# Performance work log

Hardware: AMD Instinct MI355X
Metric: run time of the kernel (lower is better)

## Reference

```python
import jax, jax.numpy as jnp
import numpy as np

B, S, D, H = 2, 2048, 1024, 16
DK = D // H

def setup_inputs() -> dict:
    key = jax.random.key(0)
    ks = jax.random.split(key, 8)
    def lin(k):
        kw, kb = jax.random.split(k)
        w = jax.random.normal(kw, (D, D), dtype=jnp.float32) / np.sqrt(D)
        b = jax.random.normal(kb, (D,), dtype=jnp.float32) * 0.01
        return w, b
    wq, bq = lin(ks[0]); wk, bk = lin(ks[1]); wv, bv = lin(ks[2]); wo, bo = lin(ks[3])
    return {
        'q': jax.random.normal(ks[4], (B, S, D), dtype=jnp.float32),
        'k': jax.random.normal(ks[5], (B, S, D), dtype=jnp.float32),
        'v': jax.random.normal(ks[6], (B, S, D), dtype=jnp.float32),
        'mask': jnp.ones((1, 1, S, S), dtype=jnp.int32),
        'wq': wq, 'bq': bq, 'wk': wk, 'bk': bk,
        'wv': wv, 'bv': bv, 'wo': wo, 'bo': bo,
    }

def reference(q, k, v, mask, wq, bq, wk, bk, wv, bv, wo, bo):
    b, s, _ = q.shape
    # QKV projections (nn.Linear: x @ W^T + b)
    Q = (q @ wq.T + bq).reshape(b, s, H, DK).transpose(0, 2, 1, 3)  # [B,H,S,DK]
    K = (k @ wk.T + bk).reshape(b, -1, H, DK).transpose(0, 2, 1, 3)
    V = (v @ wv.T + bv).reshape(b, -1, H, DK).transpose(0, 2, 1, 3)
    scores = jnp.einsum('bhqd,bhkd->bhqk', Q, K) / np.sqrt(DK)
    # faithful to source: masked positions set to -1e-09 (tiny, as written)
    scores = jnp.where(mask == 0, jnp.float32(-1e-09), scores)
    att = jax.nn.softmax(scores, axis=-1)
    x = jnp.einsum('bhqk,bhkd->bhqd', att, V)
    x = x.transpose(0, 2, 1, 3).reshape(b, s, H * DK)
    return x @ wo.T + bo
```

## Files before the change

kernel.cpp:

```cpp
#include <hip/hip_runtime.h>
#include <stdint.h>

typedef unsigned short u16;
typedef unsigned int u32;
typedef __bf16 bf16x8 __attribute__((ext_vector_type(8)));
typedef __bf16 bf16x2 __attribute__((ext_vector_type(2)));
typedef float f32x4 __attribute__((ext_vector_type(4)));
typedef float f32x16 __attribute__((ext_vector_type(16)));
typedef unsigned short u16x4 __attribute__((ext_vector_type(4)));
typedef unsigned short u16x8 __attribute__((ext_vector_type(8)));
typedef u32 u32x4 __attribute__((ext_vector_type(4)));

#define B_ 2
#define S_ 2048
#define D_ 1024
#define H_ 16

__device__ __forceinline__ u16 f2bf(float f) {
  uint32_t u = __builtin_bit_cast(uint32_t, f);
  u += 0x7FFF + ((u >> 16) & 1);
  return (u16)(u >> 16);
}

__device__ __forceinline__ u32 pkbf(float x, float y) {
  bf16x2 t;
  t.x = (__bf16)x;
  t.y = (__bf16)y;
  return __builtin_bit_cast(u32, t);
}

__device__ __forceinline__ void pl32swap(u32& a, u32& b) {
  asm("v_permlane32_swap_b32 %0, %1" : "+v"(a), "+v"(b));
}

__device__ __forceinline__ float max3f(float a, float b, float c) {
  return fmaxf(fmaxf(a, b), c);
}

__device__ __forceinline__ void gld_lds16(const void* g, void* l) {
  __builtin_amdgcn_global_load_lds((const __attribute__((address_space(1))) void*)g,
                                   (__attribute__((address_space(3))) void*)l, 16, 0, 0);
}

__global__ void cvt_w(const float* __restrict__ wq, const float* __restrict__ wk,
                      const float* __restrict__ wv, const float* __restrict__ wo,
                      u16* __restrict__ wqb, u16* __restrict__ wkb,
                      u16* __restrict__ wvb, u16* __restrict__ wob) {
  int bid = blockIdx.x;
  const float* s;
  u16* d;
  int base;
  if (bid < 1024)       { s = wq; d = wqb; base = bid; }
  else if (bid < 2048)  { s = wk; d = wkb; base = bid - 1024; }
  else if (bid < 3072)  { s = wv; d = wvb; base = bid - 2048; }
  else                  { s = wo; d = wob; base = bid - 3072; }
  int i = (base * 256 + threadIdx.x) * 4;
  float4 f = *(const float4*)(s + i);
  u16x4 o;
  o.x = f2bf(f.x); o.y = f2bf(f.y); o.z = f2bf(f.z); o.w = f2bf(f.w);
  *(u16x4*)(d + i) = o;
}

template <int EPI, bool A_FP32, int BN>
__device__ __forceinline__ void gemm_body(const void* __restrict__ Ap, const u16* __restrict__ W,
                                          const float* __restrict__ bias, void* __restrict__ Cp,
                                          float scale, int m0, int n0) {
  constexpr int K = 1024;
  constexpr int N = 1024;
  constexpr int NFR = BN / 32;
  __shared__ __align__(16) u16 As[128 * 64];
  __shared__ __align__(16) u16 Ws[BN * 64];
  const int tid = threadIdx.x;
  const int lane = tid & 63, wid = tid >> 6;
  const int wm = wid >> 1, wn = wid & 1;
  const int l15 = lane & 15, l4 = lane >> 4;

  f32x4 acc[4][NFR] = {};

  float4 areg[8];
  auto loadA = [&](int kt) {
    if (A_FP32) {
      const float* Af = (const float*)Ap;
#pragma unroll
      for (int i = 0; i < 4; ++i) {
        int c = i * 256 + tid;
        int row = c >> 3, col8 = c & 7;
        const float* src = Af + (size_t)(m0 + row) * K + kt * 64 + col8 * 8;
        areg[2 * i]     = *(const float4*)(src);
        areg[2 * i + 1] = *(const float4*)(src + 4);
      }
    }
  };
  auto writeA = [&]() {
#pragma unroll
    for (int i = 0; i < 4; ++i) {
      int c = i * 256 + tid;
      int row = c >> 3, col8 = c & 7;
      u16x8 o;
      o[0] = f2bf(areg[2 * i].x);     o[1] = f2bf(areg[2 * i].y);
      o[2] = f2bf(areg[2 * i].z);     o[3] = f2bf(areg[2 * i].w);
      o[4] = f2bf(areg[2 * i + 1].x); o[5] = f2bf(areg[2 * i + 1].y);
      o[6] = f2bf(areg[2 * i + 1].z); o[7] = f2bf(areg[2 * i + 1].w);
      *(u16x8*)((char*)As + row * 128 + ((col8 << 4) ^ ((row & 7) << 4))) = o;
    }
  };

  loadA(0);
  for (int kt = 0; kt < K / 64; ++kt) {
    __syncthreads();
    if (A_FP32) {
      writeA();
    } else {
      const u16* Ab = (const u16*)Ap;
#pragma unroll
      for (int i = 0; i < 4; ++i) {
        int c = i * 256 + tid;
        int row = c >> 3;
        int scb = ((c & 7) << 4) ^ ((row & 7) << 4);
        gld_lds16(Ab + (size_t)(m0 + row) * K + (size_t)kt * 64 + (scb >> 1),
                  (char*)As + (size_t)c * 16);
      }
    }
#pragma unroll
    for (int i = 0; i < BN / 32; ++i) {
      int c = i * 256 + tid;
      int row = c >> 3;
      int scb = ((c & 7) << 4) ^ ((row & 7) << 4);
      gld_lds16(W + (size_t)(n0 + row) * K + (size_t)kt * 64 + (scb >> 1),
                (char*)Ws + (size_t)c * 16);
    }
    if (A_FP32 && kt + 1 < K / 64) loadA(kt + 1);
    __syncthreads();
#pragma unroll
    for (int kk = 0; kk < 2; ++kk) {
      bf16x8 af[4], bfr[NFR];
#pragma unroll
      for (int m = 0; m < 4; ++m) {
        int row = wm * 64 + m * 16 + l15;
        int cb = (kk * 64 + l4 * 16) ^ ((row & 7) << 4);
        af[m] = *(const bf16x8*)((const char*)As + row * 128 + cb);
      }
#pragma unroll
      for (int n = 0; n < NFR; ++n) {
        int row = wn * (BN / 2) + n * 16 + l15;
        int cb = (kk * 64 + l4 * 16) ^ ((row & 7) << 4);
        bfr[n] = *(const bf16x8*)((const char*)Ws + row * 128 + cb);
      }
#pragma unroll
      for (int m = 0; m < 4; ++m)
#pragma unroll
        for (int n = 0; n < NFR; ++n)
          acc[m][n] = __builtin_amdgcn_mfma_f32_16x16x32_bf16(af[m], bfr[n], acc[m][n], 0, 0, 0);
    }
  }

  if (EPI == 0) {
    float* C = (float*)Cp;
#pragma unroll
    for (int m = 0; m < 4; ++m)
#pragma unroll
      for (int n = 0; n < NFR; ++n) {
        int col = n0 + wn * (BN / 2) + n * 16 + l15;
        float bval = bias[col];
#pragma unroll
        for (int j = 0; j < 4; ++j) {
          int r = m0 + wm * 64 + m * 16 + l4 * 4 + j;
          C[(size_t)r * N + col] = acc[m][n][j] + bval;
        }
      }
  } else if (EPI == 1) {
    u16* C = (u16*)Cp;
#pragma unroll
    for (int m = 0; m < 4; ++m)
#pragma unroll
      for (int n = 0; n < NFR; ++n) {
        int col = n0 + wn * (BN / 2) + n * 16 + l15;
        float bval = bias[col];
        int h = col >> 6, dk = col & 63;
#pragma unroll
        for (int j = 0; j < 4; ++j) {
          int r = m0 + wm * 64 + m * 16 + l4 * 4 + j;
          int bb = r >> 11, s = r & 2047;
          C[(((size_t)bb * H_ + h) * S_ + s) * 64 + dk] = f2bf((acc[m][n][j] + bval) * scale);
        }
      }
  } else {
    u16* C = (u16*)Cp;
#pragma unroll
    for (int m = 0; m < 4; ++m)
#pragma unroll
      for (int n = 0; n < NFR; ++n) {
        int col = n0 + wn * (BN / 2) + n * 16 + l15;
        float bval = bias[col];
        int h = col >> 6, dk = col & 63;
        int r0 = m0 + wm * 64 + m * 16 + l4 * 4;
        int bb = r0 >> 11, s0 = r0 & 2047;
        u16x4 o;
#pragma unroll
        for (int j = 0; j < 4; ++j) o[j] = f2bf(acc[m][n][j] + bval);
        *(u16x4*)(C + (((size_t)bb * H_ + h) * 64 + dk) * S_ + s0) = o;
      }
  }
}

__global__ __launch_bounds__(256) void gemm_qkv(
    const float* __restrict__ q, const float* __restrict__ k, const float* __restrict__ v,
    const u16* __restrict__ wqb, const u16* __restrict__ wkb, const u16* __restrict__ wvb,
    const float* __restrict__ bq, const float* __restrict__ bk, const float* __restrict__ bv,
    u16* __restrict__ Qp, u16* __restrict__ Kp, u16* __restrict__ VTp) {
  const int flat = blockIdx.x;
  const int nf = (flat & 7) * 96 + (flat >> 3);
  const int zz = nf >> 8, rem = nf & 255;
  const int n0 = (rem & 7) * 128, m0 = (rem >> 3) * 128;
  if (zz == 2) {
    gemm_body<2, true, 128>(v, wvb, bv, VTp, 1.0f, m0, n0);
  } else if (zz == 1) {
    gemm_body<1, true, 128>(k, wkb, bk, Kp, 1.0f, m0, n0);
  } else {
    gemm_body<1, true, 128>(q, wqb, bq, Qp, 0.1803368801111244f, m0, n0);
  }
}

__global__ __launch_bounds__(256) void gemm_out(
    const u16* __restrict__ xb, const u16* __restrict__ wob,
    const float* __restrict__ bo, float* __restrict__ out) {
  const int flat = blockIdx.x;
  const int nf = (flat & 7) * 64 + (flat >> 3);
  const int n0 = (nf & 15) * 64, m0 = (nf >> 4) * 128;
  gemm_body<0, false, 64>(xb, wob, bo, out, 1.0f, m0, n0);
}

__global__ __launch_bounds__(256, 2) void attn(
    const u16* __restrict__ Qp, const u16* __restrict__ Kp,
    const u16* __restrict__ VTp, u16* __restrict__ xb) {
  const int flat = blockIdx.x;
  const int nf = (flat & 7) * 64 + (flat >> 3);
  const int bh = nf >> 4, qt = nf & 15;
  const int b = bh >> 4, h = bh & 15;
  const size_t kbase = (size_t)bh * S_ * 64;
  const int tid = threadIdx.x, lane = tid & 63, w = tid >> 6;
  const int l31 = lane & 31, hi = lane >> 5;

  __shared__ __align__(16) u16 Ks[2][64 * 64];
  __shared__ __align__(16) u16 Vs[3][64 * 64];

  bf16x8 qf[4];
  {
    const u16* qrow = Qp + kbase + (size_t)(qt * 128 + w * 32 + l31) * 64;
#pragma unroll
    for (int kk = 0; kk < 4; ++kk)
      qf[kk] = *(const bf16x8*)(qrow + kk * 16 + hi * 8);
  }

  float m = -1e30f, lsum = 0.f;
  f32x16 xacc[2] = {};
  bf16x8 pf[4];

  auto stageK = [&](int bi, int t) {
#pragma unroll
    for (int i = 0; i < 2; ++i) {
      int c = i * 256 + tid;
      int row = c >> 3;
      int scb = (((c & 7) ^ (row & 7) ^ ((row >> 3) & 3)) << 4);
      gld_lds16(Kp + kbase + (size_t)(t * 64 + row) * 64 + (scb >> 1),
                (char*)Ks[bi] + (size_t)c * 16);
    }
  };
  auto stageV = [&](int bi, int t) {
#pragma unroll
    for (int i = 0; i < 2; ++i) {
      int c = i * 256 + tid;
      int row = c >> 3;
      int scb = (((c & 7) ^ (row & 7) ^ ((row >> 3) & 3)) << 4);
      gld_lds16(VTp + kbase + (size_t)row * S_ + t * 64 + (scb >> 1),
                (char*)Vs[bi] + (size_t)c * 16);
    }
  };

  auto pv = [&](const u16* Vb) {
    __builtin_amdgcn_s_setprio(1);
#pragma unroll
    for (int kk = 0; kk < 4; ++kk)
#pragma unroll
      for (int dn = 0; dn < 2; ++dn) {
        int row = dn * 32 + l31;
        int cb = (kk * 32 + hi * 16) ^ ((((row & 7) ^ ((row >> 3) & 3))) << 4);
        bf16x8 vf = *(const bf16x8*)((const char*)Vb + row * 128 + cb);
        xacc[dn] = __builtin_amdgcn_mfma_f32_32x32x16_bf16(pf[kk], vf, xacc[dn], 0, 0, 0);
      }
    __builtin_amdgcn_s_setprio(0);
  };

  int vprev = 2, vcur = 0, vnext = 1;
  stageK(0, 0);
  stageV(0, 0);
  for (int t = 0; t < S_ / 64; ++t) {
    __syncthreads();
    if (t + 1 < S_ / 64) {
      stageK((t + 1) & 1, t + 1);
      stageV(vnext, t + 1);
    }

    const u16* Kb = Ks[t & 1];

    f32x16 sacc[2] = {};
    __builtin_amdgcn_s_setprio(1);
#pragma unroll
    for (int kk = 0; kk < 4; ++kk)
#pragma unroll
      for (int kvt = 0; kvt < 2; ++kvt) {
        int row = kvt * 32 + l31;
        int cb = (kk * 32 + hi * 16) ^ ((((row & 7) ^ ((row >> 3) & 3))) << 4);
        bf16x8 kf = *(const bf16x8*)((const char*)Kb + row * 128 + cb);
        sacc[kvt] = __builtin_amdgcn_mfma_f32_32x32x16_bf16(kf, qf[kk], sacc[kvt], 0, 0, 0);
      }
    __builtin_amdgcn_s_setprio(0);

    if (t) pv(Vs[vprev]);

    float mx;
    {
      float t0 = max3f(sacc[0][0], sacc[0][1], sacc[0][2]);
      float t1 = max3f(sacc[0][3], sacc[0][4], sacc[0][5]);
      float t2 = max3f(sacc[0][6], sacc[0][7], sacc[0][8]);
      float t3 = max3f(sacc[0][9], sacc[0][10], sacc[0][11]);
      float t4 = max3f(sacc[0][12], sacc[0][13], sacc[0][14]);
      float t5 = max3f(sacc[0][15], sacc[1][0], sacc[1][1]);
      float t6 = max3f(sacc[1][2], sacc[1][3], sacc[1][4]);
      float t7 = max3f(sacc[1][5], sacc[1][6], sacc[1][7]);
      float t8 = max3f(sacc[1][8], sacc[1][9], sacc[1][10]);
      float t9 = max3f(sacc[1][11], sacc[1][12], sacc[1][13]);
      float ta = fmaxf(sacc[1][14], sacc[1][15]);
      float u0 = max3f(t0, t1, t2);
      float u1 = max3f(t3, t4, t5);
      float u2 = max3f(t6, t7, t8);
      float u3 = fmaxf(t9, ta);
      float x = fmaxf(max3f(u0, u1, u2), u3);
      mx = fmaxf(x, __shfl_xor(x, 32, 64));
    }

    if (__any(mx - m > 8.f)) {
      float nm = fmaxf(m, mx);
      float sc = __builtin_amdgcn_exp2f(m - nm);
      m = nm;
      lsum *= sc;
#pragma unroll
      for (int r = 0; r < 16; ++r) {
        int src = ((r & 3) + 8 * (r >> 2) + 4 * hi) | (hi << 5);
        float f = __shfl(sc, src, 64);
        xacc[0][r] *= f;
        xacc[1][r] *= f;
      }
    }

    float p[2][16];
    float sum = 0.f;
#pragma unroll
    for (int t2 = 0; t2 < 2; ++t2)
#pragma unroll
      for (int r = 0; r < 16; ++r) {
        float e = __builtin_amdgcn_exp2f(sacc[t2][r] - m);
        p[t2][r] = e;
        sum += e;
      }
    sum += __shfl_xor(sum, 32, 64);
    lsum += sum;

#pragma unroll
    for (int kk = 0; kk < 4; ++kk) {
      const int t2 = kk >> 1, rb = (kk & 1) * 8;
      u32 a0 = pkbf(p[t2][rb + 0], p[t2][rb + 1]);
      u32 a1 = pkbf(p[t2][rb + 2], p[t2][rb + 3]);
      u32 b0 = pkbf(p[t2][rb + 4], p[t2][rb + 5]);
      u32 b1 = pkbf(p[t2][rb + 6], p[t2][rb + 7]);
      pl32swap(a0, b0);
      pl32swap(a1, b1);
      u32x4 wv;
      wv.x = a0; wv.y = a1; wv.z = b0; wv.w = b1;
      pf[kk] = __builtin_bit_cast(bf16x8, wv);
    }

    vprev = vcur; vcur = vnext; vnext = (vnext + 1 == 3) ? 0 : vnext + 1;
  }

  pv(Vs[vprev]);

  float linv = 1.f / lsum;
#pragma unroll
  for (int r = 0; r < 16; ++r) {
    int qr = (r & 3) + 8 * (r >> 2) + 4 * hi;
    float f = __shfl(linv, qr | (hi << 5), 64);
    int qg = qt * 128 + w * 32 + qr;
    size_t rowb = ((size_t)b * S_ + qg) * D_ + h * 64;
    xb[rowb + l31] = f2bf(xacc[0][r] * f);
    xb[rowb + 32 + l31] = f2bf(xacc[1][r] * f);
  }
}

extern "C" void kernel_launch(void* const* d_in, const int* in_sizes, int n_in,
                              void* d_out, int out_size, void* d_ws, size_t ws_size,
                              hipStream_t stream) {
  const float* q  = (const float*)d_in[0];
  const float* k  = (const float*)d_in[1];
  const float* v  = (const float*)d_in[2];
  const float* wq = (const float*)d_in[4];
  const float* bq = (const float*)d_in[5];
  const float* wk = (const float*)d_in[6];
  const float* bk = (const float*)d_in[7];
  const float* wv = (const float*)d_in[8];
  const float* bv = (const float*)d_in[9];
  const float* wo = (const float*)d_in[10];
  const float* bo = (const float*)d_in[11];
  float* out = (float*)d_out;

  char* ws = (char*)d_ws;
  const size_t MB = 1u << 20;
  u16* wqb = (u16*)(ws + 0 * MB);
  u16* wkb = (u16*)(ws + 2 * MB);
  u16* wvb = (u16*)(ws + 4 * MB);
  u16* wob = (u16*)(ws + 6 * MB);
  u16* Qp  = (u16*)(ws + 8 * MB);
  u16* Kp  = (u16*)(ws + 16 * MB);
  u16* VTp = (u16*)(ws + 24 * MB);
  u16* xb  = (u16*)(ws + 32 * MB);

  cvt_w<<<4096, 256, 0, stream>>>(wq, wk, wv, wo, wqb, wkb, wvb, wob);
  gemm_qkv<<<768, 256, 0, stream>>>(q, k, v, wqb, wkb, wvb,
                                    bq, bk, bv, Qp, Kp, VTp);
  attn<<<512, 256, 0, stream>>>(Qp, Kp, VTp, xb);
  gemm_out<<<512, 256, 0, stream>>>(xb, wob, bo, out);
}
```

Before: 128.0 us.

## Software-pipeline QK of next tile with softmax and PV of current tile

Restructures the flash-attention main loop so that the QK^T MFMAs for tile t are issued before softmax and PV of tile t-1, using two ping-pong score accumulators (sa/sb) with a 2x manual unroll. Previously the ordering was QK(t), PV(t-1 probabilities), then softmax(t). The new order lets the exp/max VALU work of the previous tile overlap with in-flight MFMAs of the next tile. It costs extra registers for a second score buffer, which may reduce occupancy, and it makes the buffer indexing more intricate.

```diff
diff --git a/kernel.cpp b/kernel.cpp
--- a/kernel.cpp
+++ b/kernel.cpp
@@ -254,7 +254,7 @@
 
   float m = -1e30f, lsum = 0.f;
   f32x16 xacc[2] = {};
-  bf16x8 pf[4];
+  f32x16 sa[2], sb[2];
 
   auto stageK = [&](int bi, int t) {
 #pragma unroll
@@ -277,33 +277,9 @@
     }
   };
 
-  auto pv = [&](const u16* Vb) {
-    __builtin_amdgcn_s_setprio(1);
-#pragma unroll
-    for (int kk = 0; kk < 4; ++kk)
-#pragma unroll
-      for (int dn = 0; dn < 2; ++dn) {
-        int row = dn * 32 + l31;
-        int cb = (kk * 32 + hi * 16) ^ ((((row & 7) ^ ((row >> 3) & 3))) << 4);
-        bf16x8 vf = *(const bf16x8*)((const char*)Vb + row * 128 + cb);
-        xacc[dn] = __builtin_amdgcn_mfma_f32_32x32x16_bf16(pf[kk], vf, xacc[dn], 0, 0, 0);
-      }
-    __builtin_amdgcn_s_setprio(0);
-  };
-
-  int vprev = 2, vcur = 0, vnext = 1;
-  stageK(0, 0);
-  stageV(0, 0);
-  for (int t = 0; t < S_ / 64; ++t) {
-    __syncthreads();
-    if (t + 1 < S_ / 64) {
-      stageK((t + 1) & 1, t + 1);
-      stageV(vnext, t + 1);
-    }
-
-    const u16* Kb = Ks[t & 1];
-
-    f32x16 sacc[2] = {};
+  auto qk = [&](const u16* Kb, f32x16 (&s)[2]) {
+    s[0] = f32x16{};
+    s[1] = f32x16{};
     __builtin_amdgcn_s_setprio(1);
 #pragma unroll
     for (int kk = 0; kk < 4; ++kk)
@@ -312,25 +288,25 @@
         int row = kvt * 32 + l31;
         int cb = (kk * 32 + hi * 16) ^ ((((row & 7) ^ ((row >> 3) & 3))) << 4);
         bf16x8 kf = *(const bf16x8*)((const char*)Kb + row * 128 + cb);
-        sacc[kvt] = __builtin_amdgcn_mfma_f32_32x32x16_bf16(kf, qf[kk], sacc[kvt], 0, 0, 0);
+        s[kvt] = __builtin_amdgcn_mfma_f32_32x32x16_bf16(kf, qf[kk], s[kvt], 0, 0, 0);
       }
     __builtin_amdgcn_s_setprio(0);
-
-    if (t) pv(Vs[vprev]);
-
+  };
+
+  auto smpack = [&](f32x16 (&s)[2], bf16x8 (&pf)[4]) {
     float mx;
     {
-      float t0 = max3f(sacc[0][0], sacc[0][1], sacc[0][2]);
-      float t1 = max3f(sacc[0][3], sacc[0][4], sacc[0][5]);
-      float t2 = max3f(sacc[0][6], sacc[0][7], sacc[0][8]);
-      float t3 = max3f(sacc[0][9], sacc[0][10], sacc[0][11]);
-      float t4 = max3f(sacc[0][12], sacc[0][13], sacc[0][14]);
-      float t5 = max3f(sacc[0][15], sacc[1][0], sacc[1][1]);
-      float t6 = max3f(sacc[1][2], sacc[1][3], sacc[1][4]);
-      float t7 = max3f(sacc[1][5], sacc[1][6], sacc[1][7]);
-      float t8 = max3f(sacc[1][8], sacc[1][9], sacc[1][10]);
-      float t9 = max3f(sacc[1][11], sacc[1][12], sacc[1][13]);
-      float ta = fmaxf(sacc[1][14], sacc[1][15]);
+      float t0 = max3f(s[0][0], s[0][1], s[0][2]);
+      float t1 = max3f(s[0][3], s[0][4], s[0][5]);
+      float t2 = max3f(s[0][6], s[0][7], s[0][8]);
+      float t3 = max3f(s[0][9], s[0][10], s[0][11]);
+      float t4 = max3f(s[0][12], s[0][13], s[0][14]);
+      float t5 = max3f(s[0][15], s[1][0], s[1][1]);
+      float t6 = max3f(s[1][2], s[1][3], s[1][4]);
+      float t7 = max3f(s[1][5], s[1][6], s[1][7]);
+      float t8 = max3f(s[1][8], s[1][9], s[1][10]);
+      float t9 = max3f(s[1][11], s[1][12], s[1][13]);
+      float ta = fmaxf(s[1][14], s[1][15]);
       float u0 = max3f(t0, t1, t2);
       float u1 = max3f(t3, t4, t5);
       float u2 = max3f(t6, t7, t8);
@@ -359,7 +335,7 @@
     for (int t2 = 0; t2 < 2; ++t2)
 #pragma unroll
       for (int r = 0; r < 16; ++r) {
-        float e = __builtin_amdgcn_exp2f(sacc[t2][r] - m);
+        float e = __builtin_amdgcn_exp2f(s[t2][r] - m);
         p[t2][r] = e;
         sum += e;
       }
@@ -379,11 +355,66 @@
       wv.x = a0; wv.y = a1; wv.z = b0; wv.w = b1;
       pf[kk] = __builtin_bit_cast(bf16x8, wv);
     }
-
-    vprev = vcur; vcur = vnext; vnext = (vnext + 1 == 3) ? 0 : vnext + 1;
-  }
-
-  pv(Vs[vprev]);
+  };
+
+  auto pv = [&](const u16* Vb, bf16x8 (&pf)[4]) {
+    __builtin_amdgcn_s_setprio(1);
+#pragma unroll
+    for (int kk = 0; kk < 4; ++kk)
+#pragma unroll
+      for (int dn = 0; dn < 2; ++dn) {
+        int row = dn * 32 + l31;
+        int cb = (kk * 32 + hi * 16) ^ ((((row & 7) ^ ((row >> 3) & 3))) << 4);
+        bf16x8 vf = *(const bf16x8*)((const char*)Vb + row * 128 + cb);
+        xacc[dn] = __builtin_amdgcn_mfma_f32_32x32x16_bf16(pf[kk], vf, xacc[dn], 0, 0, 0);
+      }
+    __builtin_amdgcn_s_setprio(0);
+  };
+
+  stageK(0, 0);
+  stageV(0, 0);
+  __syncthreads();
+  stageK(1, 1);
+  stageV(1, 1);
+  qk(Ks[0], sa);
+
+  int vm1 = 0;
+#pragma unroll 1
+  for (int t = 1; t < 31; t += 2) {
+    {
+      __syncthreads();
+      stageK((t + 1) & 1, t + 1);
+      stageV((t + 1) % 3, t + 1);
+      qk(Ks[t & 1], sb);
+      bf16x8 pf[4];
+      smpack(sa, pf);
+      pv(Vs[vm1], pf);
+      vm1 = (vm1 + 1 == 3) ? 0 : vm1 + 1;
+    }
+    {
+      __syncthreads();
+      stageK(t & 1, t + 2);
+      stageV((t + 2) % 3, t + 2);
+      qk(Ks[(t + 1) & 1], sa);
+      bf16x8 pf[4];
+      smpack(sb, pf);
+      pv(Vs[vm1], pf);
+      vm1 = (vm1 + 1 == 3) ? 0 : vm1 + 1;
+    }
+  }
+  {
+    __syncthreads();
+    qk(Ks[1], sb);
+    bf16x8 pf[4];
+    smpack(sa, pf);
+    pv(Vs[vm1], pf);
+    vm1 = (vm1 + 1 == 3) ? 0 : vm1 + 1;
+  }
+  {
+    bf16x8 pf[4];
+    smpack(sb, pf);
+    pv(Vs[vm1], pf);
+  }
 
   float linv = 1.f / lsum;
 #pragma unroll
```

Result: no change. 129.3 us (+1.0%).
